# Kernel tuning notes

Hardware: AMD Instinct MI355X
Metric: run time of the kernel (lower is better)

## Reference

```python
import jax, jax.numpy as jnp
import numpy as np

B, P, D = 64, 196, 768
HP = WP = 14
N_CLASSES = 200
C = N_CLASSES + 1
K_PROTO = 5
GAMMA = 0.999
TEMP = 0.2
EPS_SK = 0.05
SK_ITERS = 3


def l2norm(x, axis=-1, eps=1e-12):
    n = jnp.linalg.norm(x, axis=axis, keepdims=True)
    return x / jnp.maximum(n, eps)


def _safe_div(a, b):
    return a / jnp.where(b > 0, b, 1.0)


def masked_sinkhorn(L_cnk, mask):
    """Vectorized per-class Sinkhorn-Knopp over masked patch groups.
    L_cnk: [C, N, K] logits; mask: [C, N] bool (patch n belongs to class c).
    Returns Q: [C, K, N] (columns of each present class sum to 1)."""
    m = mask[:, None, :].astype(L_cnk.dtype)  # [C,1,N]
    Q = jnp.exp(jnp.transpose(L_cnk, (0, 2, 1)) / EPS_SK) * m  # [C,K,N]
    Q = _safe_div(Q, Q.sum(axis=(1, 2), keepdims=True))
    Nc = mask.sum(axis=1).astype(Q.dtype)[:, None, None]  # per-class patch count
    Nc_safe = jnp.where(Nc > 0, Nc, 1.0)
    for _ in range(SK_ITERS):
        Q = _safe_div(Q, Q.sum(axis=2, keepdims=True)) / K_PROTO  # row (prototype) norm
        Q = _safe_div(Q, Q.sum(axis=1, keepdims=True)) / Nc_safe  # col (patch) norm
    Q = Q * Nc  # undo final /Nc -> each patch column sums to 1
    return Q


def setup_inputs() -> dict:
    key = jax.random.key(0)
    k1, k2, k3, k4, k5 = jax.random.split(key, 5)
    patch_tokens = jax.random.normal(k1, (B, P, D), dtype=jnp.float32)
    raw_patch_tokens = jax.random.normal(k2, (B, P, D), dtype=jnp.float32)
    prototypes = 0.02 * jax.random.normal(k3, (C, K_PROTO, D), dtype=jnp.float32)
    sa_weights = jnp.full((N_CLASSES, K_PROTO), 0.5, dtype=jnp.float32)
    pseudo_patch_labels = jax.random.randint(k5, (B, HP, WP), 0, C, dtype=jnp.int32)
    return {
        "patch_tokens": patch_tokens,
        "raw_patch_tokens": raw_patch_tokens,
        "prototypes": prototypes,
        "sa_weights": sa_weights,
        "pseudo_patch_labels": pseudo_patch_labels,
    }


def reference(patch_tokens, raw_patch_tokens, prototypes, sa_weights, pseudo_patch_labels):
    # --- patch-prototype cosine similarity ---
    pt = l2norm(patch_tokens)                       # [B,P,D]
    proto_n = l2norm(prototypes)                    # [C,K,D]
    logits = jnp.einsum('bpd,ckd->bpck', pt, proto_n)  # [B,P,C,K]
    image_logits = logits.max(axis=1)               # [B,C,K]
    # --- ScoreAggregation classifier ---
    sw = jax.nn.softmax(sa_weights, axis=-1) * K_PROTO  # [n_classes,K]
    class_logits = (image_logits[:, :-1, :] * sw).sum(-1) / TEMP  # [B,n_classes]
    # --- online clustering (detached in original) ---
    rpt = l2norm(raw_patch_tokens)
    patches_flat = rpt.reshape(-1, D)               # [N,D], N=B*P
    labels_flat = pseudo_patch_labels.reshape(-1)   # [N]
    N = labels_flat.shape[0]
    L_nck = logits.reshape(N, C, K_PROTO)
    L_cnk = jnp.transpose(L_nck, (1, 0, 2))         # [C,N,K]
    mask = labels_flat[None, :] == jnp.arange(C)[:, None]  # [C,N]
    Q = masked_sinkhorn(L_cnk, mask)                # [C,K,N]
    # grouped GEMM: P_c_new = Q_c @ I_c for every class at once
    P_new_c = jnp.einsum('ckn,nd->ckd', Q, patches_flat)  # [C,K,D]
    present = mask.any(axis=1)[:, None, None]
    P_new = jnp.where(present,
                      GAMMA * prototypes + (1.0 - GAMMA) * P_new_c,
                      prototypes)
    # part assignment: argmax_k Q[label_n, k, n] + label_n * K
    Q_nck = jnp.transpose(Q, (2, 0, 1))             # [N,C,K]
    Q_at = Q_nck[jnp.arange(N), labels_flat]        # [N,K]
    assign = jnp.argmax(Q_at, axis=-1).astype(jnp.int32) + labels_flat * K_PROTO
    part_assignment_maps = assign.reshape(B, HP * WP)
    return (logits, image_logits, class_logits, part_assignment_maps, P_new)
```

## Files before the change

kernel.cpp:

```cpp
#include <hip/hip_runtime.h>
#include <math.h>

#define B_ 64
#define P_ 196
#define D_ 768
#define C_ 201
#define K_ 5
#define N_ (B_*P_)
#define CK_ (C_*K_)
#define NPAD 1024
#define NCLS 200
#define GAMMA_ 0.999f
#define INV_TEMP 5.0f
#define INV_EPS 20.0f
#define CAP2 256
#define MTILES 98
#define ROWS_TOT (2*N_ + NPAD)

typedef short s16x8 __attribute__((ext_vector_type(8)));
typedef float f32x4 __attribute__((ext_vector_type(4)));
typedef unsigned short u16x4 __attribute__((ext_vector_type(4)));

typedef __attribute__((address_space(3))) void lds_void;
typedef __attribute__((address_space(1))) const void g_void;
#define GLD16(gp, lp) __builtin_amdgcn_global_load_lds((g_void*)(gp), (lds_void*)(lp), 16, 0, 0)

__device__ __forceinline__ unsigned short f2bf(float f) {
    unsigned int u = __float_as_uint(f);
    unsigned int r = (u + 0x7FFFu + ((u >> 16) & 1u)) >> 16;
    return (unsigned short)r;
}

__global__ __launch_bounds__(256) void norm_all_kernel(
        const float* __restrict__ patch, const float* __restrict__ rawp,
        const float* __restrict__ proto, float* __restrict__ invR,
        unsigned short* __restrict__ Abf, unsigned short* __restrict__ Bbf,
        int* __restrict__ cnt) {
    if (blockIdx.x == 0 && threadIdx.x < C_) cnt[threadIdx.x] = 0;
    int gw = blockIdx.x * 4 + (threadIdx.x >> 6);
    int lane = threadIdx.x & 63;
    const float* src; unsigned short* dst; int realR; int r; bool wantInv = false;
    if (gw < N_) { r = gw; src = patch; dst = Abf; realR = N_; }
    else if (gw < 2 * N_) { r = gw - N_; src = rawp; dst = nullptr; realR = N_; wantInv = true; }
    else { r = gw - 2 * N_; src = proto; dst = Bbf; realR = CK_; }
    unsigned short* brow = dst ? dst + (size_t)r * D_ : nullptr;
    if (r >= realR) {
        u16x4 z = (u16x4)0;
        *(u16x4*)(brow + lane * 4)       = z;
        *(u16x4*)(brow + lane * 4 + 256) = z;
        *(u16x4*)(brow + lane * 4 + 512) = z;
        return;
    }
    const float4* row4 = (const float4*)(src + (size_t)r * D_);
    float4 v0 = row4[lane], v1 = row4[lane + 64], v2 = row4[lane + 128];
    float s = v0.x*v0.x + v0.y*v0.y + v0.z*v0.z + v0.w*v0.w
            + v1.x*v1.x + v1.y*v1.y + v1.z*v1.z + v1.w*v1.w
            + v2.x*v2.x + v2.y*v2.y + v2.z*v2.z + v2.w*v2.w;
#pragma unroll
    for (int o = 1; o < 64; o <<= 1) s += __shfl_xor(s, o, 64);
    float sc = 1.f / fmaxf(sqrtf(s), 1e-12f);
    if (brow) {
        u16x4 p0 = { f2bf(v0.x*sc), f2bf(v0.y*sc), f2bf(v0.z*sc), f2bf(v0.w*sc) };
        u16x4 p1 = { f2bf(v1.x*sc), f2bf(v1.y*sc), f2bf(v1.z*sc), f2bf(v1.w*sc) };
        u16x4 p2 = { f2bf(v2.x*sc), f2bf(v2.y*sc), f2bf(v2.z*sc), f2bf(v2.w*sc) };
        *(u16x4*)(brow + lane * 4)       = p0;
        *(u16x4*)(brow + lane * 4 + 256) = p1;
        *(u16x4*)(brow + lane * 4 + 512) = p2;
    } else if (wantInv && lane == 0) invR[r] = sc;
}

#define BM 128
#define BN 128
#define BKq 32
__global__ __launch_bounds__(256) void gemm_mfma_kernel(
    const unsigned short* __restrict__ Ab, const unsigned short* __restrict__ Bb,
    float* __restrict__ Cc,
    float* __restrict__ part) {
    __shared__ short As[2][BM * BKq];
    __shared__ short Bs[2][BN * BKq];
    __shared__ float maxw[4][2][BN];
    int tid = threadIdx.x;
    int bid = blockIdx.y * 8 + blockIdx.x;
    int swz = (bid & 7) * MTILES + (bid >> 3);
    int mtile = swz >> 3;
    int ntile = swz & 7;
    int mBase = mtile * BM;
    int nBase = ntile * BN;
    int w = tid >> 6;
    int lane = tid & 63;
    int wm = (w >> 1) * 64;
    int wn = (w & 1) * 64;
    int mrow = lane & 15;
    int kq = (lane >> 4) * 8;

    f32x4 acc[4][4];
#pragma unroll
    for (int i = 0; i < 4; ++i)
#pragma unroll
        for (int j = 0; j < 4; ++j) acc[i][j] = (f32x4)(0.f);

    int c0 = tid, c1 = tid + 256;
    const unsigned short* ga0 = Ab + (size_t)(mBase + (c0 >> 2)) * D_ + (c0 & 3) * 8;
    const unsigned short* ga1 = Ab + (size_t)(mBase + (c1 >> 2)) * D_ + (c1 & 3) * 8;
    const unsigned short* gb0 = Bb + (size_t)(nBase + (c0 >> 2)) * D_ + (c0 & 3) * 8;
    const unsigned short* gb1 = Bb + (size_t)(nBase + (c1 >> 2)) * D_ + (c1 & 3) * 8;

    auto stage = [&](int buf, int k0) {
        GLD16(ga0 + k0, &As[buf][c0 * 8]);
        GLD16(ga1 + k0, &As[buf][c1 * 8]);
        GLD16(gb0 + k0, &Bs[buf][c0 * 8]);
        GLD16(gb1 + k0, &Bs[buf][c1 * 8]);
    };

    stage(0, 0);
    __syncthreads();
    int cur = 0;
    for (int k0 = 0; k0 < D_; k0 += BKq) {
        int nk = k0 + BKq;
        if (nk < D_) stage(cur ^ 1, nk);
        s16x8 a[4], b[4];
#pragma unroll
        for (int i = 0; i < 4; ++i)
            a[i] = *(const s16x8*)&As[cur][(wm + 16 * i + mrow) * BKq + kq];
#pragma unroll
        for (int j = 0; j < 4; ++j)
            b[j] = *(const s16x8*)&Bs[cur][(wn + 16 * j + mrow) * BKq + kq];
#pragma unroll
        for (int i = 0; i < 4; ++i)
#pragma unroll
            for (int j = 0; j < 4; ++j)
                acc[i][j] = __builtin_amdgcn_mfma_f32_16x16x32_bf16(a[i], b[j], acc[i][j], 0, 0, 0);
        __syncthreads();
        cur ^= 1;
    }

#pragma unroll
    for (int i = 0; i < 4; ++i) {
        int gm = mBase + wm + 16 * i + (lane >> 4) * 4;
#pragma unroll
        for (int j = 0; j < 4; ++j) {
            int gn = nBase + wn + 16 * j + (lane & 15);
            if (gn < CK_) {
                Cc[(size_t)(gm + 0) * CK_ + gn] = acc[i][j][0];
                Cc[(size_t)(gm + 1) * CK_ + gn] = acc[i][j][1];
                Cc[(size_t)(gm + 2) * CK_ + gn] = acc[i][j][2];
                Cc[(size_t)(gm + 3) * CK_ + gn] = acc[i][j][3];
            }
        }
    }

    int imgA = mBase / 196;
    int rstar = 196 * (imgA + 1);
#pragma unroll
    for (int j = 0; j < 4; ++j) {
        float m0 = -INFINITY, m1 = -INFINITY;
#pragma unroll
        for (int i = 0; i < 4; ++i) {
            int gm = mBase + wm + 16 * i + (lane >> 4) * 4;
#pragma unroll
            for (int r = 0; r < 4; ++r) {
                float v = acc[i][j][r];
                if (gm + r >= rstar) m1 = fmaxf(m1, v); else m0 = fmaxf(m0, v);
            }
        }
        m0 = fmaxf(m0, __shfl_xor(m0, 16)); m0 = fmaxf(m0, __shfl_xor(m0, 32));
        m1 = fmaxf(m1, __shfl_xor(m1, 16)); m1 = fmaxf(m1, __shfl_xor(m1, 32));
        if (lane < 16) {
            maxw[w][0][wn + 16 * j + lane] = m0;
            maxw[w][1][wn + 16 * j + lane] = m1;
        }
    }
    __syncthreads();
    int s = tid >> 7, col = tid & 127, h = col >> 6;
    float vmax = fmaxf(maxw[h][s][col], maxw[h + 2][s][col]);
    part[(size_t)(mtile * 2 + s) * 1024 + nBase + col] = vmax;
}

__global__ void imgcls_kernel(const float* __restrict__ part, const float* __restrict__ saw,
                              float* __restrict__ img, float* __restrict__ cls) {
    __shared__ float simg[CK_];
    int b = blockIdx.x;
    int t0 = (196 * b) >> 7;
    int t1 = (196 * b + 195) >> 7;
    for (int n = threadIdx.x; n < CK_; n += 256) {
        float m = -INFINITY;
        for (int t = t0; t <= t1; ++t) {
            int iA = (t << 7) / 196;
            int s = (iA == b) ? 0 : 1;
            m = fmaxf(m, part[(size_t)(t * 2 + s) * 1024 + n]);
        }
        img[b * CK_ + n] = m;
        simg[n] = m;
    }
    __syncthreads();
    int c = threadIdx.x;
    if (c < NCLS) {
        float w[K_];
        float mx = -INFINITY;
#pragma unroll
        for (int k = 0; k < K_; ++k) { w[k] = saw[c * K_ + k]; mx = fmaxf(mx, w[k]); }
        float ssum = 0.f;
#pragma unroll
        for (int k = 0; k < K_; ++k) { w[k] = expf(w[k] - mx); ssum += w[k]; }
        float acc = 0.f;
#pragma unroll
        for (int k = 0; k < K_; ++k)
            acc += simg[c * K_ + k] * (w[k] / ssum * (float)K_);
        cls[b * NCLS + c] = acc * INV_TEMP;
    }
}

__global__ void compact_kernel(const float* __restrict__ L, const int* __restrict__ labels,
                               int* __restrict__ cnt, int* __restrict__ idxList,
                               float* __restrict__ EList) {
    int n = blockIdx.x * 256 + threadIdx.x;
    if (n >= N_) return;
    int c = labels[n];
    int slot = atomicAdd(&cnt[c], 1);
    if (slot < CAP2) {
        idxList[c * CAP2 + slot] = n;
        const float* lp = L + (size_t)n * CK_ + c * K_;
#pragma unroll
        for (int k = 0; k < K_; ++k)
            EList[((size_t)(c * K_ + k)) * CAP2 + slot] = expf(lp[k] * INV_EPS);
    }
}

#define NJ (CAP2/64)
__global__ __launch_bounds__(256) void sinkhorn_kernel(
    const int* __restrict__ cnt, const int* __restrict__ idxList,
    const float* __restrict__ EList, const float* __restrict__ invR,
    float* __restrict__ WList, float* __restrict__ outAssign) {
    int c = blockIdx.x * 4 + (threadIdx.x >> 6);
    if (c >= C_) return;
    int lane = threadIdx.x & 63;
    int Nc = cnt[c]; if (Nc > CAP2) Nc = CAP2;
    if (Nc == 0) return;
    float e[NJ][K_];
    float cn[NJ];
    int idx[NJ];
#pragma unroll
    for (int j = 0; j < NJ; ++j) {
        int n = j * 64 + lane;
        bool v = n < Nc;
        cn[j] = v ? 1.f : 0.f;
        idx[j] = v ? idxList[c * CAP2 + n] : 0;
#pragma unroll
        for (int k = 0; k < K_; ++k)
            e[j][k] = v ? EList[((size_t)(c * K_ + k)) * CAP2 + n] : 0.f;
    }
    float r[K_];
    for (int it = 0; it < 3; ++it) {
#pragma unroll
        for (int k = 0; k < K_; ++k) {
            float s = 0.f;
#pragma unroll
            for (int j = 0; j < NJ; ++j) s += e[j][k] * cn[j];
            for (int o = 32; o > 0; o >>= 1) s += __shfl_xor(s, o, 64);
            r[k] = 1.f / ((float)K_ * s);
        }
#pragma unroll
        for (int j = 0; j < NJ; ++j) {
            float t = 0.f;
#pragma unroll
            for (int k = 0; k < K_; ++k) t += e[j][k] * r[k];
            cn[j] = (j * 64 + lane < Nc) ? 1.f / ((float)Nc * t) : 0.f;
        }
    }
#pragma unroll
    for (int j = 0; j < NJ; ++j) {
        int n = j * 64 + lane;
        if (n >= Nc) continue;
        int kb = 0; float best = e[j][0] * r[0];
#pragma unroll
        for (int k = 1; k < K_; ++k) {
            float v = e[j][k] * r[k];
            if (v > best) { best = v; kb = k; }
        }
        outAssign[idx[j]] = (float)(kb + c * K_);
        float scale = cn[j] * (float)Nc * (1.0f - GAMMA_) * invR[idx[j]];
#pragma unroll
        for (int k = 0; k < K_; ++k)
            WList[((size_t)(c * K_ + k)) * CAP2 + n] = e[j][k] * r[k] * scale;
    }
}

__global__ __launch_bounds__(192) void ema_kernel(
    const int* __restrict__ cnt, const int* __restrict__ idxList,
    const float* __restrict__ WList, const float* __restrict__ rawP,
    const float* __restrict__ proto, float* __restrict__ outProto) {
    int c = blockIdx.x;
    int d = blockIdx.y * 192 + threadIdx.x;
    int Nc = cnt[c]; if (Nc > CAP2) Nc = CAP2;
    size_t protoOff = (size_t)c * K_ * D_;
    if (Nc == 0) {
#pragma unroll
        for (int k = 0; k < K_; ++k)
            outProto[protoOff + (size_t)k * D_ + d] = proto[protoOff + (size_t)k * D_ + d];
        return;
    }
    __shared__ int s_idx[CAP2];
    __shared__ float s_w[K_][CAP2];
    for (int i = threadIdx.x; i < Nc; i += 192) {
        s_idx[i] = idxList[c * CAP2 + i];
#pragma unroll
        for (int k = 0; k < K_; ++k) s_w[k][i] = WList[((size_t)(c * K_ + k)) * CAP2 + i];
    }
    __syncthreads();
    float acc[K_] = {};
    int n = 0;
    for (; n + 1 < Nc; n += 2) {
        float v0 = rawP[(size_t)s_idx[n] * D_ + d];
        float v1 = rawP[(size_t)s_idx[n + 1] * D_ + d];
#pragma unroll
        for (int k = 0; k < K_; ++k) {
            acc[k] = fmaf(s_w[k][n], v0, acc[k]);
            acc[k] = fmaf(s_w[k][n + 1], v1, acc[k]);
        }
    }
    if (n < Nc) {
        float v0 = rawP[(size_t)s_idx[n] * D_ + d];
#pragma unroll
        for (int k = 0; k < K_; ++k) acc[k] = fmaf(s_w[k][n], v0, acc[k]);
    }
#pragma unroll
    for (int k = 0; k < K_; ++k)
        outProto[protoOff + (size_t)k * D_ + d] =
            fmaf(GAMMA_, proto[protoOff + (size_t)k * D_ + d], acc[k]);
}

extern "C" void kernel_launch(void* const* d_in, const int* in_sizes, int n_in,
                              void* d_out, int out_size, void* d_ws, size_t ws_size,
                              hipStream_t stream) {
    (void)in_sizes; (void)n_in; (void)out_size; (void)ws_size;
    const float* patch  = (const float*)d_in[0];
    const float* rawp   = (const float*)d_in[1];
    const float* proto  = (const float*)d_in[2];
    const float* saw    = (const float*)d_in[3];
    const int*   labels = (const int*)d_in[4];

    float* out    = (float*)d_out;
    float* logits = out;
    float* img    = out + 12606720;
    float* cls    = out + 12671040;
    float* assign = out + 12683840;
    float* pnew   = out + 12696384;

    float* ws   = (float*)d_ws;
    float* invR = ws;
    unsigned short* Abf = (unsigned short*)(ws + N_);
    unsigned short* Bbf = Abf + (size_t)N_ * D_;
    int*   cnt     = (int*)(Bbf + (size_t)NPAD * D_);
    int*   idxList = cnt + 256;
    float* EList   = (float*)(idxList + C_ * CAP2);
    float* WList   = EList + (size_t)C_ * K_ * CAP2;
    float* part    = WList + (size_t)C_ * K_ * CAP2;

    norm_all_kernel<<<ROWS_TOT / 4, 256, 0, stream>>>(patch, rawp, proto, invR, Abf, Bbf, cnt);
    gemm_mfma_kernel<<<dim3(NPAD / BN, MTILES), 256, 0, stream>>>(Abf, Bbf, logits, part);
    imgcls_kernel<<<B_, 256, 0, stream>>>(part, saw, img, cls);
    compact_kernel<<<(N_ + 255) / 256, 256, 0, stream>>>(logits, labels, cnt, idxList, EList);
    sinkhorn_kernel<<<(C_ + 3) / 4, 256, 0, stream>>>(cnt, idxList, EList, invR, WList, assign);
    ema_kernel<<<dim3(C_, 4), 192, 0, stream>>>(cnt, idxList, WList, rawp, proto, pnew);
}
```

Before: 202.2 us.

## Triple-buffer GEMM loads and fuse post-processing kernels into two launches

The GEMM main loop moves from double to triple buffering, using explicit vmcnt waits and a single barrier per iteration so loads run two stages ahead. The image/class reduction and the compaction kernels are merged into one launch, and Sinkhorn is fused with the EMA prototype update so the weights stay in shared memory. This removes two kernel launches and a global round trip for the weights. In exchange, the fused EMA uses one block per class (201 blocks instead of 804), so parallelism is lower and that stage sits on one wave's Sinkhorn. The hand-written waitcnt depends on the exact number of outstanding loads.

Result: faster. 190.5 us (-5.8%).

```diff
diff --git a/kernel.cpp b/kernel.cpp
--- a/kernel.cpp
+++ b/kernel.cpp
@@ -72,12 +72,14 @@
 #define BM 128
 #define BN 128
 #define BKq 32
+#define KITER (D_/BKq)
+#define NBUF 3
 __global__ __launch_bounds__(256) void gemm_mfma_kernel(
     const unsigned short* __restrict__ Ab, const unsigned short* __restrict__ Bb,
     float* __restrict__ Cc,
     float* __restrict__ part) {
-    __shared__ short As[2][BM * BKq];
-    __shared__ short Bs[2][BN * BKq];
+    __shared__ short As[NBUF][BM * BKq];
+    __shared__ short Bs[NBUF][BN * BKq];
     __shared__ float maxw[4][2][BN];
     int tid = threadIdx.x;
     int bid = blockIdx.y * 8 + blockIdx.x;
@@ -113,25 +115,27 @@
     };
 
     stage(0, 0);
-    __syncthreads();
-    int cur = 0;
-    for (int k0 = 0; k0 < D_; k0 += BKq) {
-        int nk = k0 + BKq;
-        if (nk < D_) stage(cur ^ 1, nk);
+    stage(1, BKq);
+    for (int u = 0; u < KITER; ++u) {
+        if (u < KITER - 1) asm volatile("s_waitcnt vmcnt(4)" ::: "memory");
+        else               asm volatile("s_waitcnt vmcnt(0)" ::: "memory");
+        __builtin_amdgcn_s_barrier();
+        __builtin_amdgcn_sched_barrier(0);
+        if (u + 2 < KITER) stage((u + 2) % NBUF, (u + 2) * BKq);
+        const short* Ac = As[u % NBUF];
+        const short* Bc = Bs[u % NBUF];
         s16x8 a[4], b[4];
 #pragma unroll
         for (int i = 0; i < 4; ++i)
-            a[i] = *(const s16x8*)&As[cur][(wm + 16 * i + mrow) * BKq + kq];
+            a[i] = *(const s16x8*)&Ac[(wm + 16 * i + mrow) * BKq + kq];
 #pragma unroll
         for (int j = 0; j < 4; ++j)
-            b[j] = *(const s16x8*)&Bs[cur][(wn + 16 * j + mrow) * BKq + kq];
+            b[j] = *(const s16x8*)&Bc[(wn + 16 * j + mrow) * BKq + kq];
 #pragma unroll
         for (int i = 0; i < 4; ++i)
 #pragma unroll
             for (int j = 0; j < 4; ++j)
                 acc[i][j] = __builtin_amdgcn_mfma_f32_16x16x32_bf16(a[i], b[j], acc[i][j], 0, 0, 0);
-        __syncthreads();
-        cur ^= 1;
     }
 
 #pragma unroll
@@ -176,157 +180,147 @@
     part[(size_t)(mtile * 2 + s) * 1024 + nBase + col] = vmax;
 }
 
-__global__ void imgcls_kernel(const float* __restrict__ part, const float* __restrict__ saw,
-                              float* __restrict__ img, float* __restrict__ cls) {
+__global__ __launch_bounds__(256) void post_kernel(
+        const float* __restrict__ part, const float* __restrict__ saw,
+        float* __restrict__ img, float* __restrict__ cls,
+        const float* __restrict__ L, const int* __restrict__ labels,
+        int* __restrict__ cnt, int* __restrict__ idxList, float* __restrict__ EList) {
     __shared__ float simg[CK_];
-    int b = blockIdx.x;
-    int t0 = (196 * b) >> 7;
-    int t1 = (196 * b + 195) >> 7;
-    for (int n = threadIdx.x; n < CK_; n += 256) {
-        float m = -INFINITY;
-        for (int t = t0; t <= t1; ++t) {
-            int iA = (t << 7) / 196;
-            int s = (iA == b) ? 0 : 1;
-            m = fmaxf(m, part[(size_t)(t * 2 + s) * 1024 + n]);
-        }
-        img[b * CK_ + n] = m;
-        simg[n] = m;
-    }
-    __syncthreads();
-    int c = threadIdx.x;
-    if (c < NCLS) {
-        float w[K_];
-        float mx = -INFINITY;
-#pragma unroll
-        for (int k = 0; k < K_; ++k) { w[k] = saw[c * K_ + k]; mx = fmaxf(mx, w[k]); }
-        float ssum = 0.f;
-#pragma unroll
-        for (int k = 0; k < K_; ++k) { w[k] = expf(w[k] - mx); ssum += w[k]; }
-        float acc = 0.f;
-#pragma unroll
-        for (int k = 0; k < K_; ++k)
-            acc += simg[c * K_ + k] * (w[k] / ssum * (float)K_);
-        cls[b * NCLS + c] = acc * INV_TEMP;
-    }
-}
-
-__global__ void compact_kernel(const float* __restrict__ L, const int* __restrict__ labels,
-                               int* __restrict__ cnt, int* __restrict__ idxList,
-                               float* __restrict__ EList) {
-    int n = blockIdx.x * 256 + threadIdx.x;
-    if (n >= N_) return;
-    int c = labels[n];
-    int slot = atomicAdd(&cnt[c], 1);
-    if (slot < CAP2) {
-        idxList[c * CAP2 + slot] = n;
-        const float* lp = L + (size_t)n * CK_ + c * K_;
-#pragma unroll
-        for (int k = 0; k < K_; ++k)
-            EList[((size_t)(c * K_ + k)) * CAP2 + slot] = expf(lp[k] * INV_EPS);
+    if (blockIdx.x < B_) {
+        int b = blockIdx.x;
+        int t0 = (196 * b) >> 7;
+        int t1 = (196 * b + 195) >> 7;
+        for (int n = threadIdx.x; n < CK_; n += 256) {
+            float m = -INFINITY;
+            for (int t = t0; t <= t1; ++t) {
+                int iA = (t << 7) / 196;
+                int s = (iA == b) ? 0 : 1;
+                m = fmaxf(m, part[(size_t)(t * 2 + s) * 1024 + n]);
+            }
+            img[b * CK_ + n] = m;
+            simg[n] = m;
+        }
+        __syncthreads();
+        int c = threadIdx.x;
+        if (c < NCLS) {
+            float w[K_];
+            float mx = -INFINITY;
+#pragma unroll
+            for (int k = 0; k < K_; ++k) { w[k] = saw[c * K_ + k]; mx = fmaxf(mx, w[k]); }
+            float ssum = 0.f;
+#pragma unroll
+            for (int k = 0; k < K_; ++k) { w[k] = expf(w[k] - mx); ssum += w[k]; }
+            float acc = 0.f;
+#pragma unroll
+            for (int k = 0; k < K_; ++k)
+                acc += simg[c * K_ + k] * (w[k] / ssum * (float)K_);
+            cls[b * NCLS + c] = acc * INV_TEMP;
+        }
+    } else {
+        int n = (blockIdx.x - B_) * 256 + threadIdx.x;
+        if (n >= N_) return;
+        int c = labels[n];
+        int slot = atomicAdd(&cnt[c], 1);
+        if (slot < CAP2) {
+            idxList[c * CAP2 + slot] = n;
+            const float* lp = L + (size_t)n * CK_ + c * K_;
+#pragma unroll
+            for (int k = 0; k < K_; ++k)
+                EList[((size_t)(c * K_ + k)) * CAP2 + slot] = expf(lp[k] * INV_EPS);
+        }
     }
 }
 
 #define NJ (CAP2/64)
-__global__ __launch_bounds__(256) void sinkhorn_kernel(
+__global__ __launch_bounds__(256) void sinkema_kernel(
     const int* __restrict__ cnt, const int* __restrict__ idxList,
     const float* __restrict__ EList, const float* __restrict__ invR,
-    float* __restrict__ WList, float* __restrict__ outAssign) {
-    int c = blockIdx.x * 4 + (threadIdx.x >> 6);
-    if (c >= C_) return;
-    int lane = threadIdx.x & 63;
-    int Nc = cnt[c]; if (Nc > CAP2) Nc = CAP2;
-    if (Nc == 0) return;
-    float e[NJ][K_];
-    float cn[NJ];
-    int idx[NJ];
-#pragma unroll
-    for (int j = 0; j < NJ; ++j) {
-        int n = j * 64 + lane;
-        bool v = n < Nc;
-        cn[j] = v ? 1.f : 0.f;
-        idx[j] = v ? idxList[c * CAP2 + n] : 0;
-#pragma unroll
-        for (int k = 0; k < K_; ++k)
-            e[j][k] = v ? EList[((size_t)(c * K_ + k)) * CAP2 + n] : 0.f;
-    }
-    float r[K_];
-    for (int it = 0; it < 3; ++it) {
-#pragma unroll
-        for (int k = 0; k < K_; ++k) {
-            float s = 0.f;
-#pragma unroll
-            for (int j = 0; j < NJ; ++j) s += e[j][k] * cn[j];
-            for (int o = 32; o > 0; o >>= 1) s += __shfl_xor(s, o, 64);
-            r[k] = 1.f / ((float)K_ * s);
-        }
-#pragma unroll
-        for (int j = 0; j < NJ; ++j) {
-            float t = 0.f;
-#pragma unroll
-            for (int k = 0; k < K_; ++k) t += e[j][k] * r[k];
-            cn[j] = (j * 64 + lane < Nc) ? 1.f / ((float)Nc * t) : 0.f;
-        }
-    }
-#pragma unroll
-    for (int j = 0; j < NJ; ++j) {
-        int n = j * 64 + lane;
-        if (n >= Nc) continue;
-        int kb = 0; float best = e[j][0] * r[0];
-#pragma unroll
-        for (int k = 1; k < K_; ++k) {
-            float v = e[j][k] * r[k];
-            if (v > best) { best = v; kb = k; }
-        }
-        outAssign[idx[j]] = (float)(kb + c * K_);
-        float scale = cn[j] * (float)Nc * (1.0f - GAMMA_) * invR[idx[j]];
-#pragma unroll
-        for (int k = 0; k < K_; ++k)
-            WList[((size_t)(c * K_ + k)) * CAP2 + n] = e[j][k] * r[k] * scale;
-    }
-}
-
-__global__ __launch_bounds__(192) void ema_kernel(
-    const int* __restrict__ cnt, const int* __restrict__ idxList,
-    const float* __restrict__ WList, const float* __restrict__ rawP,
-    const float* __restrict__ proto, float* __restrict__ outProto) {
+    const float* __restrict__ rawP, const float* __restrict__ proto,
+    float* __restrict__ outAssign, float* __restrict__ outProto) {
     int c = blockIdx.x;
-    int d = blockIdx.y * 192 + threadIdx.x;
+    int tid = threadIdx.x;
     int Nc = cnt[c]; if (Nc > CAP2) Nc = CAP2;
     size_t protoOff = (size_t)c * K_ * D_;
     if (Nc == 0) {
-#pragma unroll
-        for (int k = 0; k < K_; ++k)
-            outProto[protoOff + (size_t)k * D_ + d] = proto[protoOff + (size_t)k * D_ + d];
+        for (int i = tid; i < K_ * D_; i += 256)
+            outProto[protoOff + i] = proto[protoOff + i];
         return;
     }
+    __shared__ float s_w[K_][CAP2];
     __shared__ int s_idx[CAP2];
-    __shared__ float s_w[K_][CAP2];
-    for (int i = threadIdx.x; i < Nc; i += 192) {
-        s_idx[i] = idxList[c * CAP2 + i];
-#pragma unroll
-        for (int k = 0; k < K_; ++k) s_w[k][i] = WList[((size_t)(c * K_ + k)) * CAP2 + i];
+    for (int i = tid; i < CAP2; i += 256)
+        s_idx[i] = (i < Nc) ? idxList[c * CAP2 + i] : 0;
+
+    if (tid < 64) {
+        int lane = tid;
+        float e[NJ][K_];
+        float cn[NJ];
+#pragma unroll
+        for (int j = 0; j < NJ; ++j) {
+            int n = j * 64 + lane;
+            bool v = n < Nc;
+            cn[j] = v ? 1.f : 0.f;
+#pragma unroll
+            for (int k = 0; k < K_; ++k)
+                e[j][k] = v ? EList[((size_t)(c * K_ + k)) * CAP2 + n] : 0.f;
+        }
+        float r[K_];
+        for (int it = 0; it < 3; ++it) {
+#pragma unroll
+            for (int k = 0; k < K_; ++k) {
+                float s = 0.f;
+#pragma unroll
+                for (int j = 0; j < NJ; ++j) s += e[j][k] * cn[j];
+                for (int o = 32; o > 0; o >>= 1) s += __shfl_xor(s, o, 64);
+                r[k] = 1.f / ((float)K_ * s);
+            }
+#pragma unroll
+            for (int j = 0; j < NJ; ++j) {
+                float t = 0.f;
+#pragma unroll
+                for (int k = 0; k < K_; ++k) t += e[j][k] * r[k];
+                cn[j] = (j * 64 + lane < Nc) ? 1.f / ((float)Nc * t) : 0.f;
+            }
+        }
+#pragma unroll
+        for (int j = 0; j < NJ; ++j) {
+            int n = j * 64 + lane;
+            if (n >= Nc) continue;
+            int idxn = idxList[c * CAP2 + n];
+            int kb = 0; float best = e[j][0] * r[0];
+#pragma unroll
+            for (int k = 1; k < K_; ++k) {
+                float v = e[j][k] * r[k];
+                if (v > best) { best = v; kb = k; }
+            }
+            outAssign[idxn] = (float)(kb + c * K_);
+            float scale = cn[j] * (float)Nc * (1.0f - GAMMA_) * invR[idxn];
+#pragma unroll
+            for (int k = 0; k < K_; ++k)
+                s_w[k][n] = e[j][k] * r[k] * scale;
+        }
     }
     __syncthreads();
-    float acc[K_] = {};
-    int n = 0;
-    for (; n + 1 < Nc; n += 2) {
-        float v0 = rawP[(size_t)s_idx[n] * D_ + d];
-        float v1 = rawP[(size_t)s_idx[n + 1] * D_ + d];
+
+    float a0[K_] = {}, a1[K_] = {}, a2[K_] = {};
+    for (int n = 0; n < Nc; ++n) {
+        const float* rp = rawP + (size_t)s_idx[n] * D_;
+        float v0 = rp[tid], v1 = rp[tid + 256], v2 = rp[tid + 512];
 #pragma unroll
         for (int k = 0; k < K_; ++k) {
-            acc[k] = fmaf(s_w[k][n], v0, acc[k]);
-            acc[k] = fmaf(s_w[k][n + 1], v1, acc[k]);
-        }
-    }
-    if (n < Nc) {
-        float v0 = rawP[(size_t)s_idx[n] * D_ + d];
-#pragma unroll
-        for (int k = 0; k < K_; ++k) acc[k] = fmaf(s_w[k][n], v0, acc[k]);
-    }
-#pragma unroll
-    for (int k = 0; k < K_; ++k)
-        outProto[protoOff + (size_t)k * D_ + d] =
-            fmaf(GAMMA_, proto[protoOff + (size_t)k * D_ + d], acc[k]);
+            float wv = s_w[k][n];
+            a0[k] = fmaf(wv, v0, a0[k]);
+            a1[k] = fmaf(wv, v1, a1[k]);
+            a2[k] = fmaf(wv, v2, a2[k]);
+        }
+    }
+#pragma unroll
+    for (int k = 0; k < K_; ++k) {
+        size_t o = protoOff + (size_t)k * D_;
+        outProto[o + tid]       = fmaf(GAMMA_, proto[o + tid],       a0[k]);
+        outProto[o + tid + 256] = fmaf(GAMMA_, proto[o + tid + 256], a1[k]);
+        outProto[o + tid + 512] = fmaf(GAMMA_, proto[o + tid + 512], a2[k]);
+    }
 }
 
 extern "C" void kernel_launch(void* const* d_in, const int* in_sizes, int n_in,
@@ -358,8 +352,8 @@
 
     norm_all_kernel<<<ROWS_TOT / 4, 256, 0, stream>>>(patch, rawp, proto, invR, Abf, Bbf, cnt);
     gemm_mfma_kernel<<<dim3(NPAD / BN, MTILES), 256, 0, stream>>>(Abf, Bbf, logits, part);
-    imgcls_kernel<<<B_, 256, 0, stream>>>(part, saw, img, cls);
-    compact_kernel<<<(N_ + 255) / 256, 256, 0, stream>>>(logits, labels, cnt, idxList, EList);
-    sinkhorn_kernel<<<(C_ + 3) / 4, 256, 0, stream>>>(cnt, idxList, EList, invR, WList, assign);
-    ema_kernel<<<dim3(C_, 4), 192, 0, stream>>>(cnt, idxList, WList, rawp, proto, pnew);
-}
+    post_kernel<<<B_ + N_ / 256, 256, 0, stream>>>(part, saw, img, cls, logits, labels,
+                                                   cnt, idxList, EList);
+    sinkema_kernel<<<C_, 256, 0, stream>>>(cnt, idxList, EList, invR, rawp, proto,
+                                           assign, pnew);
+}
```
